# Kernel tuning notes

Hardware: AMD Instinct MI355X
Metric: run time of the kernel (lower is better)

## Reference

```python
import jax, jax.numpy as jnp
import numpy as np

N, M, D = 1024, 1024, 512


def setup_inputs() -> dict:
    key = jax.random.key(0)
    ks = jax.random.split(key, 12)
    s = 1.0 / np.sqrt(D)
    return {
        "q": jax.random.normal(ks[0], (N, D), jnp.float32),
        "k": jax.random.normal(ks[1], (M, D), jnp.float32),
        "v": jax.random.normal(ks[2], (M, D), jnp.float32),
        "mask": jax.random.randint(ks[3], (N, M), 0, 2) > 0,
        "Wq": jax.random.normal(ks[4], (D, D), jnp.float32) * s,
        "bq": jax.random.normal(ks[5], (D,), jnp.float32) * s,
        "Wk": jax.random.normal(ks[6], (D, D), jnp.float32) * s,
        "bk": jax.random.normal(ks[7], (D,), jnp.float32) * s,
        "Wv": jax.random.normal(ks[8], (D, D), jnp.float32) * s,
        "bv": jax.random.normal(ks[9], (D,), jnp.float32) * s,
        "Ww": jax.random.normal(ks[10], (D,), jnp.float32) * s,
        "bw": jax.random.normal(ks[11], (1,), jnp.float32) * s,
    }


def reference(q, k, v, mask, Wq, bq, Wk, bk, Wv, bv, Ww, bw):
    # Linear projections (torch Linear: x @ W.T + b)
    qp = q @ Wq.T + bq  # [N, D]
    kp = k @ Wk.T + bk  # [M, D]
    vp = v @ Wv.T + bv  # [M, D]
    # Bahdanau additive score: W(tanh(q_n + k_m)) -> [N, M]
    h = jnp.tanh(qp[:, None, :] + kp[None, :, :])  # [N, M, D]
    scores = jnp.einsum('nmd,d->nm', h, Ww) + bw[0]
    scores = jnp.where(mask, scores, jnp.float32(-1000000.0))
    attn = jax.nn.softmax(scores, axis=1)  # softmax over M (dim 1)
    context = jnp.einsum('nm,md->nd', attn, vp)  # [N, D]
    return context
```

## Files before the change

kernel.cpp:

```cpp
#include <hip/hip_runtime.h>
#include <hip/hip_bf16.h>
#include <float.h>


#define NROWS 1024
#define DDIM  512
#define MDIM  1024

typedef __attribute__((ext_vector_type(8))) short s8v;
typedef __attribute__((ext_vector_type(4))) float f4v;
typedef __attribute__((ext_vector_type(2))) float v2f;

__device__ __forceinline__ float bf2f(ushort h) {
    return __uint_as_float(((unsigned)h) << 16);
}
__device__ __forceinline__ ushort2 f2bf2(float a, float b) {
    __hip_bfloat162 t = __float22bfloat162_rn(float2{a, b});
    union { __hip_bfloat162 v; ushort2 u; } c; c.v = t;
    return c.u;
}
__device__ __forceinline__ void hl2(float a, float b, ushort2& h, ushort2& l) {
    h = f2bf2(a, b);
    l = f2bf2(a - bf2f(h.x), b - bf2f(h.y));
}

__global__ __launch_bounds__(256) void proj_gemm(
    const float* __restrict__ q, const float* __restrict__ kk_,
    const float* __restrict__ v,
    const float* __restrict__ Wq, const float* __restrict__ bq,
    const float* __restrict__ Wk, const float* __restrict__ bk,
    const float* __restrict__ Wv, const float* __restrict__ bv,
    float* __restrict__ eq, float* __restrict__ ekT,
    ushort* __restrict__ vph, ushort* __restrict__ vpl,
    float* __restrict__ rsum, float CS)
{
    __shared__ ushort Ah[4096], Al[4096], Bh[4096], Bl[4096];

    const float* A; const float* B; const float* bias;
    int biasRow;
    if (blockIdx.z == 0)      { A = q;   B = Wq;  bias = bq; biasRow = 0; }
    else if (blockIdx.z == 1) { A = Wk;  B = kk_; bias = bk; biasRow = 1; }
    else                      { A = Wv;  B = v;   bias = bv; biasRow = 1; }

    const int bi = (blockIdx.z == 0) ? blockIdx.x : blockIdx.y;
    const int bj = (blockIdx.z == 0) ? blockIdx.y : blockIdx.x;

    const int t    = threadIdx.x;
    const int lane = t & 63;
    const int w    = t >> 6;
    const int lm   = lane & 15;
    const int lq   = lane >> 4;
    const int i0   = bi * 64;
    const int j0   = bj * 64;
    const int mh   = (w >> 1) * 32;
    const int nh   = (w & 1) * 32;

    if (blockIdx.z == 0 && blockIdx.x == 0 && blockIdx.y == 0) {
        float4 zz = {0.f, 0.f, 0.f, 0.f};
        *(float4*)&rsum[t * 4] = zz;
    }

    f4v acc[2][2] = {{{0.f,0.f,0.f,0.f},{0.f,0.f,0.f,0.f}},
                     {{0.f,0.f,0.f,0.f},{0.f,0.f,0.f,0.f}}};
    float4 pa[4], pb[4];

    const int sr = t >> 4, sc4 = t & 15;
#pragma unroll
    for (int p = 0; p < 4; ++p) {
        int r = sr + p * 16;
        pa[p] = *(const float4*)&A[(size_t)(i0 + r) * DDIM + sc4 * 4];
        pb[p] = *(const float4*)&B[(size_t)(j0 + r) * DDIM + sc4 * 4];
    }

    for (int kc = 0; kc < 8; ++kc) {
        __syncthreads();
#pragma unroll
        for (int p = 0; p < 4; ++p) {
            int r = sr + p * 16;
            int ad = r * 64 + (((sc4 >> 1) ^ (r & 7)) << 3) + (sc4 & 1) * 4;
            ushort2 h01, l01, h23, l23;
            hl2(pa[p].x, pa[p].y, h01, l01);
            hl2(pa[p].z, pa[p].w, h23, l23);
            ushort4 ha = {h01.x, h01.y, h23.x, h23.y};
            ushort4 la = {l01.x, l01.y, l23.x, l23.y};
            *(ushort4*)&Ah[ad] = ha;
            *(ushort4*)&Al[ad] = la;
            hl2(pb[p].x, pb[p].y, h01, l01);
            hl2(pb[p].z, pb[p].w, h23, l23);
            ushort4 hb = {h01.x, h01.y, h23.x, h23.y};
            ushort4 lb = {l01.x, l01.y, l23.x, l23.y};
            *(ushort4*)&Bh[ad] = hb;
            *(ushort4*)&Bl[ad] = lb;
        }
        __syncthreads();
        if (kc < 7) {
            const int k0 = (kc + 1) * 64;
#pragma unroll
            for (int p = 0; p < 4; ++p) {
                int r = sr + p * 16;
                pa[p] = *(const float4*)&A[(size_t)(i0 + r) * DDIM + k0 + sc4 * 4];
                pb[p] = *(const float4*)&B[(size_t)(j0 + r) * DDIM + k0 + sc4 * 4];
            }
        }
#pragma unroll
        for (int ks = 0; ks < 2; ++ks) {
            const int kb = ks * 4 + lq;
            s8v afh[2], afl[2], bfh[2], bfl[2];
#pragma unroll
            for (int g = 0; g < 2; ++g) {
                int ra = mh + g * 16 + lm;
                int rb = nh + g * 16 + lm;
                int aa = ra * 64 + ((kb ^ (ra & 7)) << 3);
                int ab = rb * 64 + ((kb ^ (rb & 7)) << 3);
                afh[g] = *(const s8v*)&Ah[aa];
                afl[g] = *(const s8v*)&Al[aa];
                bfh[g] = *(const s8v*)&Bh[ab];
                bfl[g] = *(const s8v*)&Bl[ab];
            }
#pragma unroll
            for (int mi = 0; mi < 2; ++mi)
#pragma unroll
                for (int ni = 0; ni < 2; ++ni) {
                    acc[mi][ni] = __builtin_amdgcn_mfma_f32_16x16x32_bf16(
                        afh[mi], bfh[ni], acc[mi][ni], 0, 0, 0);
                    acc[mi][ni] = __builtin_amdgcn_mfma_f32_16x16x32_bf16(
                        afh[mi], bfl[ni], acc[mi][ni], 0, 0, 0);
                    acc[mi][ni] = __builtin_amdgcn_mfma_f32_16x16x32_bf16(
                        afl[mi], bfh[ni], acc[mi][ni], 0, 0, 0);
                }
        }
    }

    const float CLAMP = 8192.0f;
    const float SCw   = 1.220703125e-4f;
#pragma unroll
    for (int mi = 0; mi < 2; ++mi) {
#pragma unroll
        for (int ni = 0; ni < 2; ++ni) {
#pragma unroll
            for (int p = 0; p < 4; ++p) {
                int row = i0 + mh + mi * 16 + lq * 4 + p;
                int col = j0 + nh + ni * 16 + lm;
                float val = acc[mi][ni][p] + (biasRow ? bias[row] : bias[col]);
                if (blockIdx.z == 0) {
                    eq[(size_t)row * 512 + col] =
                        fminf(__builtin_amdgcn_exp2f(val * CS), CLAMP) * SCw;
                } else if (blockIdx.z == 1) {
                    ekT[(size_t)row * 1024 + col] =
                        fminf(__builtin_amdgcn_exp2f(val * CS), CLAMP);
                } else {
                    ushort2 h2 = f2bf2(val, val);
                    vph[(size_t)row * 1024 + col] = h2.x;
                    ushort2 l2 = f2bf2(val - bf2f(h2.x), 0.f);
                    vpl[(size_t)row * 1024 + col] = l2.x;
                }
            }
        }
    }
}


#define TREE8(K0,K1,K2,K3,K4,K5,K6,K7,DCQ)                                     \
    {                                                                          \
        float4 wgA = *(const float4*)&wws[(DCQ)];                              \
        float4 wgB = *(const float4*)&wws[(DCQ) + 4];                          \
        _Pragma("unroll")                                                      \
        for (int nn = 0; nn < 4; ++nn) {                                       \
            float4 egA = *(const float4*)&es[nn * 512 + (DCQ)];                \
            float4 egB = *(const float4*)&es[nn * 512 + (DCQ) + 4];            \
            v2f A0 = __builtin_elementwise_fma(K0, (v2f){egA.x, egA.x}, cc2);  \
            v2f A1 = __builtin_elementwise_fma(K1, (v2f){egA.y, egA.y}, cc2);  \
            v2f A2 = __builtin_elementwise_fma(K2, (v2f){egA.z, egA.z}, cc2);  \
            v2f A3 = __builtin_elementwise_fma(K3, (v2f){egA.w, egA.w}, cc2);  \
            v2f A4 = __builtin_elementwise_fma(K4, (v2f){egB.x, egB.x}, cc2);  \
            v2f A5 = __builtin_elementwise_fma(K5, (v2f){egB.y, egB.y}, cc2);  \
            v2f A6 = __builtin_elementwise_fma(K6, (v2f){egB.z, egB.z}, cc2);  \
            v2f A7 = __builtin_elementwise_fma(K7, (v2f){egB.w, egB.w}, cc2);  \
            v2f n01 = __builtin_elementwise_fma((v2f){wgA.y, wgA.y}, A0,       \
                                                (v2f){wgA.x, wgA.x} * A1);     \
            v2f d01 = A0 * A1;                                                 \
            v2f n23 = __builtin_elementwise_fma((v2f){wgA.w, wgA.w}, A2,       \
                                                (v2f){wgA.z, wgA.z} * A3);     \
            v2f d23 = A2 * A3;                                                 \
            v2f n45 = __builtin_elementwise_fma((v2f){wgB.y, wgB.y}, A4,       \
                                                (v2f){wgB.x, wgB.x} * A5);     \
            v2f d45 = A4 * A5;                                                 \
            v2f n67 = __builtin_elementwise_fma((v2f){wgB.w, wgB.w}, A6,       \
                                                (v2f){wgB.z, wgB.z} * A7);     \
            v2f d67 = A6 * A7;                                                 \
            v2f nA = __builtin_elementwise_fma(n01, d23, n23 * d01);           \
            v2f dA = d01 * d23;                                                \
            v2f nB = __builtin_elementwise_fma(n45, d67, n67 * d45);           \
            v2f dB = d45 * d67;                                                \
            v2f num = __builtin_elementwise_fma(nA, dB, nB * dA);              \
            v2f den = dA * dB;                                                 \
            v2f r = {__builtin_amdgcn_rcpf(den.x),                             \
                     __builtin_amdgcn_rcpf(den.y)};                            \
            acc[nn] = __builtin_elementwise_fma(num, r, acc[nn]);              \
        }                                                                      \
    }

__global__ __launch_bounds__(256) void score_kernel(const float* __restrict__ eq,
                                                    const float* __restrict__ ekT,
                                                    const float* __restrict__ Ww,
                                                    const int* __restrict__ mask,
                                                    ushort* __restrict__ Ph,
                                                    ushort* __restrict__ Pl,
                                                    float* __restrict__ rsum)
{
    __shared__ __align__(16) float es[4 * 512];
    __shared__ __align__(16) float wws[512];
    const int t    = threadIdx.x;
    const int lane = t & 63;
    const int w    = t >> 6;
    const int mw   = blockIdx.x * 512 + w * 128;
    const int n0   = blockIdx.y * 4;

    const float SC = 1.220703125e-4f;

#pragma unroll
    for (int p = 0; p < 2; ++p) {
        int idx = t + p * 256;
        int nl = idx >> 7, c4 = idx & 127;
        *(float4*)&es[nl * 512 + c4 * 4] =
            *(const float4*)&eq[(size_t)(n0 + nl) * DDIM + c4 * 4];
    }
    wws[t]       = Ww[t] * SC;
    wws[t + 256] = Ww[t + 256] * SC;

    const float* gk = ekT + mw + lane * 2;

    v2f a0 = *(const v2f*)(gk + (size_t)0 * MDIM);
    v2f a1 = *(const v2f*)(gk + (size_t)1 * MDIM);
    v2f a2 = *(const v2f*)(gk + (size_t)2 * MDIM);
    v2f a3 = *(const v2f*)(gk + (size_t)3 * MDIM);
    v2f a4 = *(const v2f*)(gk + (size_t)4 * MDIM);
    v2f a5 = *(const v2f*)(gk + (size_t)5 * MDIM);
    v2f a6 = *(const v2f*)(gk + (size_t)6 * MDIM);
    v2f a7 = *(const v2f*)(gk + (size_t)7 * MDIM);

    __syncthreads();

    v2f acc[4] = {};
    const v2f cc2 = {1.220703125e-4f, 1.220703125e-4f};

    for (int dc = 0; dc < 512; dc += 16) {
        const float* g8 = gk + (size_t)(dc + 8) * MDIM;
        v2f b0 = *(const v2f*)(g8 + (size_t)0 * MDIM);
        v2f b1 = *(const v2f*)(g8 + (size_t)1 * MDIM);
        v2f b2 = *(const v2f*)(g8 + (size_t)2 * MDIM);
        v2f b3 = *(const v2f*)(g8 + (size_t)3 * MDIM);
        v2f b4 = *(const v2f*)(g8 + (size_t)4 * MDIM);
        v2f b5 = *(const v2f*)(g8 + (size_t)5 * MDIM);
        v2f b6 = *(const v2f*)(g8 + (size_t)6 * MDIM);
        v2f b7 = *(const v2f*)(g8 + (size_t)7 * MDIM);

        TREE8(a0, a1, a2, a3, a4, a5, a6, a7, dc)

        if (dc + 16 < 512) {
            const float* g16 = gk + (size_t)(dc + 16) * MDIM;
            a0 = *(const v2f*)(g16 + (size_t)0 * MDIM);
            a1 = *(const v2f*)(g16 + (size_t)1 * MDIM);
            a2 = *(const v2f*)(g16 + (size_t)2 * MDIM);
            a3 = *(const v2f*)(g16 + (size_t)3 * MDIM);
            a4 = *(const v2f*)(g16 + (size_t)4 * MDIM);
            a5 = *(const v2f*)(g16 + (size_t)5 * MDIM);
            a6 = *(const v2f*)(g16 + (size_t)6 * MDIM);
            a7 = *(const v2f*)(g16 + (size_t)7 * MDIM);
        }

        TREE8(b0, b1, b2, b3, b4, b5, b6, b7, dc + 8)
    }

    const float C2 = -2.8853900817779268f;
    const int m = mw + lane * 2;
    float rs[4];
#pragma unroll
    for (int nn = 0; nn < 4; ++nn) {
        int n = n0 + nn;
        int2 mk = *(const int2*)&mask[(size_t)n * MDIM + m];
        float p0 = mk.x ? __builtin_amdgcn_exp2f(acc[nn].x * C2) : 0.f;
        float p1 = mk.y ? __builtin_amdgcn_exp2f(acc[nn].y * C2) : 0.f;
        ushort2 h, l;
        hl2(p0, p1, h, l);
        *(ushort2*)&Ph[(size_t)n * MDIM + m] = h;
        *(ushort2*)&Pl[(size_t)n * MDIM + m] = l;
        rs[nn] = p0 + p1;
    }
#pragma unroll
    for (int off = 32; off; off >>= 1) {
        rs[0] += __shfl_xor(rs[0], off);
        rs[1] += __shfl_xor(rs[1], off);
        rs[2] += __shfl_xor(rs[2], off);
        rs[3] += __shfl_xor(rs[3], off);
    }
    if (lane == 0) {
#pragma unroll
        for (int nn = 0; nn < 4; ++nn)
            atomicAdd(&rsum[n0 + nn], rs[nn]);
    }
}

__global__ __launch_bounds__(256) void ctx_gemm(const ushort* __restrict__ Ph,
                                                const ushort* __restrict__ Pl,
                                                const ushort* __restrict__ vph,
                                                const ushort* __restrict__ vpl,
                                                const float* __restrict__ rsum,
                                                float* __restrict__ out)
{
    __shared__ __align__(16) float red[3 * 64 * 4];
    const int t    = threadIdx.x;
    const int lane = t & 63;
    const int w    = t >> 6;
    const int lm   = lane & 15;
    const int lq   = lane >> 4;
    const int d0   = blockIdx.x * 16;
    const int n0   = blockIdx.y * 16;
    const int mb   = w * 256;

    const ushort* pAh = Ph  + (size_t)(n0 + lm) * MDIM + mb + lq * 8;
    const ushort* pAl = Pl  + (size_t)(n0 + lm) * MDIM + mb + lq * 8;
    const ushort* pBh = vph + (size_t)(d0 + lm) * MDIM + mb + lq * 8;
    const ushort* pBl = vpl + (size_t)(d0 + lm) * MDIM + mb + lq * 8;

    f4v acc = {0.f, 0.f, 0.f, 0.f};
#pragma unroll 4
    for (int m0 = 0; m0 < 256; m0 += 32) {
        s8v ah = *(const s8v*)(pAh + m0);
        s8v al = *(const s8v*)(pAl + m0);
        s8v bh = *(const s8v*)(pBh + m0);
        s8v bl = *(const s8v*)(pBl + m0);
        acc = __builtin_amdgcn_mfma_f32_16x16x32_bf16(ah, bh, acc, 0, 0, 0);
        acc = __builtin_amdgcn_mfma_f32_16x16x32_bf16(ah, bl, acc, 0, 0, 0);
        acc = __builtin_amdgcn_mfma_f32_16x16x32_bf16(al, bh, acc, 0, 0, 0);
    }

    if (w > 0) *(f4v*)&red[((w - 1) * 64 + lane) * 4] = acc;
    __syncthreads();
    if (w == 0) {
#pragma unroll
        for (int i = 0; i < 3; ++i)
            acc += *(const f4v*)&red[(i * 64 + lane) * 4];
#pragma unroll
        for (int p = 0; p < 4; ++p) {
            int nrow = n0 + lq * 4 + p;
            float inv = __builtin_amdgcn_rcpf(rsum[nrow]);
            out[(size_t)nrow * DDIM + d0 + lm] = acc[p] * inv;
        }
    }
}

extern "C" void kernel_launch(void* const* d_in, const int* in_sizes, int n_in,
                              void* d_out, int out_size, void* d_ws, size_t ws_size,
                              hipStream_t stream)
{
    const float* q    = (const float*)d_in[0];
    const float* k    = (const float*)d_in[1];
    const float* v    = (const float*)d_in[2];
    const int*   mask = (const int*)d_in[3];
    const float* Wq   = (const float*)d_in[4];
    const float* bq   = (const float*)d_in[5];
    const float* Wk   = (const float*)d_in[6];
    const float* bk   = (const float*)d_in[7];
    const float* Wv   = (const float*)d_in[8];
    const float* bv   = (const float*)d_in[9];
    const float* Ww   = (const float*)d_in[10];

    float* ws    = (float*)d_ws;
    float* eq    = ws;
    float* ekT   = ws + 524288;
    ushort* vph  = (ushort*)(ws + 1048576);
    ushort* vpl  = (ushort*)(ws + 1310720);
    ushort* Ph   = (ushort*)(ws + 1572864);
    ushort* Pl   = (ushort*)(ws + 2097152);
    float* rsum  = ws + 2621440;
    float* out   = (float*)d_out;

    const float CS = 2.8853900817779268f;

    proj_gemm<<<dim3(16, 8, 3), dim3(256), 0, stream>>>(q, k, v, Wq, bq, Wk, bk,
                                                        Wv, bv, eq, ekT,
                                                        vph, vpl, rsum, CS);
    score_kernel<<<dim3(2, 256), dim3(256), 0, stream>>>(eq, ekT, Ww, mask,
                                                         Ph, Pl, rsum);
    ctx_gemm<<<dim3(32, 64), dim3(256), 0, stream>>>(Ph, Pl, vph, vpl, rsum, out);
}
```

Measured before the change: 176.1 us.

## Split score kernel's D reduction across four wavefront groups with LDS reduce

The score kernel now uses 512-thread blocks in which eight waves cover two 128-wide M groups times four 128-wide D slices. Each wave reduces only its quarter of D, and partial accumulators are combined through shared memory before the masked exp, bf16 split and row-sum atomics. Grid width doubles to 4x256 blocks, raising the number of waves to hide latency on the long serial D loop. In exchange it adds an LDS reduction, a block barrier, and idle waves during the epilogue.

```diff
diff --git a/kernel.cpp b/kernel.cpp
--- a/kernel.cpp
+++ b/kernel.cpp
@@ -200,7 +200,7 @@
         }                                                                      \
     }
 
-__global__ __launch_bounds__(256) void score_kernel(const float* __restrict__ eq,
+__global__ __launch_bounds__(512) void score_kernel(const float* __restrict__ eq,
                                                     const float* __restrict__ ekT,
                                                     const float* __restrict__ Ww,
                                                     const int* __restrict__ mask,
@@ -210,25 +210,26 @@
 {
     __shared__ __align__(16) float es[4 * 512];
     __shared__ __align__(16) float wws[512];
+    __shared__ __align__(16) float red[3 * 2 * 64 * 8];
     const int t    = threadIdx.x;
     const int lane = t & 63;
     const int w    = t >> 6;
-    const int mw   = blockIdx.x * 512 + w * 128;
+    const int mg   = w & 1;
+    const int dh   = w >> 1;
+    const int mw   = blockIdx.x * 256 + mg * 128;
     const int n0   = blockIdx.y * 4;
+    const int db   = dh * 128;
 
     const float SC = 1.220703125e-4f;
 
-#pragma unroll
-    for (int p = 0; p < 2; ++p) {
-        int idx = t + p * 256;
-        int nl = idx >> 7, c4 = idx & 127;
+    {
+        int nl = t >> 7, c4 = t & 127;
         *(float4*)&es[nl * 512 + c4 * 4] =
             *(const float4*)&eq[(size_t)(n0 + nl) * DDIM + c4 * 4];
     }
-    wws[t]       = Ww[t] * SC;
-    wws[t + 256] = Ww[t + 256] * SC;
-
-    const float* gk = ekT + mw + lane * 2;
+    wws[t] = Ww[t] * SC;
+
+    const float* gk = ekT + (size_t)db * MDIM + mw + lane * 2;
 
     v2f a0 = *(const v2f*)(gk + (size_t)0 * MDIM);
     v2f a1 = *(const v2f*)(gk + (size_t)1 * MDIM);
@@ -244,7 +245,7 @@
     v2f acc[4] = {};
     const v2f cc2 = {1.220703125e-4f, 1.220703125e-4f};
 
-    for (int dc = 0; dc < 512; dc += 16) {
+    for (int dc = 0; dc < 128; dc += 16) {
         const float* g8 = gk + (size_t)(dc + 8) * MDIM;
         v2f b0 = *(const v2f*)(g8 + (size_t)0 * MDIM);
         v2f b1 = *(const v2f*)(g8 + (size_t)1 * MDIM);
@@ -255,9 +256,9 @@
         v2f b6 = *(const v2f*)(g8 + (size_t)6 * MDIM);
         v2f b7 = *(const v2f*)(g8 + (size_t)7 * MDIM);
 
-        TREE8(a0, a1, a2, a3, a4, a5, a6, a7, dc)
-
-        if (dc + 16 < 512) {
+        TREE8(a0, a1, a2, a3, a4, a5, a6, a7, db + dc)
+
+        if (dc + 16 < 128) {
             const float* g16 = gk + (size_t)(dc + 16) * MDIM;
             a0 = *(const v2f*)(g16 + (size_t)0 * MDIM);
             a1 = *(const v2f*)(g16 + (size_t)1 * MDIM);
@@ -269,35 +270,54 @@
             a7 = *(const v2f*)(g16 + (size_t)7 * MDIM);
         }
 
-        TREE8(b0, b1, b2, b3, b4, b5, b6, b7, dc + 8)
-    }
-
-    const float C2 = -2.8853900817779268f;
-    const int m = mw + lane * 2;
-    float rs[4];
-#pragma unroll
-    for (int nn = 0; nn < 4; ++nn) {
-        int n = n0 + nn;
-        int2 mk = *(const int2*)&mask[(size_t)n * MDIM + m];
-        float p0 = mk.x ? __builtin_amdgcn_exp2f(acc[nn].x * C2) : 0.f;
-        float p1 = mk.y ? __builtin_amdgcn_exp2f(acc[nn].y * C2) : 0.f;
-        ushort2 h, l;
-        hl2(p0, p1, h, l);
-        *(ushort2*)&Ph[(size_t)n * MDIM + m] = h;
-        *(ushort2*)&Pl[(size_t)n * MDIM + m] = l;
-        rs[nn] = p0 + p1;
-    }
-#pragma unroll
-    for (int off = 32; off; off >>= 1) {
-        rs[0] += __shfl_xor(rs[0], off);
-        rs[1] += __shfl_xor(rs[1], off);
-        rs[2] += __shfl_xor(rs[2], off);
-        rs[3] += __shfl_xor(rs[3], off);
-    }
-    if (lane == 0) {
-#pragma unroll
-        for (int nn = 0; nn < 4; ++nn)
-            atomicAdd(&rsum[n0 + nn], rs[nn]);
+        TREE8(b0, b1, b2, b3, b4, b5, b6, b7, db + dc + 8)
+    }
+
+    if (dh > 0) {
+        float* rb = &red[(((dh - 1) * 2 + mg) * 64 + lane) * 8];
+        *(v2f*)&rb[0] = acc[0];
+        *(v2f*)&rb[2] = acc[1];
+        *(v2f*)&rb[4] = acc[2];
+        *(v2f*)&rb[6] = acc[3];
+    }
+    __syncthreads();
+    if (dh == 0) {
+#pragma unroll
+        for (int i = 0; i < 3; ++i) {
+            const float* rb = &red[((i * 2 + mg) * 64 + lane) * 8];
+            acc[0] += *(const v2f*)&rb[0];
+            acc[1] += *(const v2f*)&rb[2];
+            acc[2] += *(const v2f*)&rb[4];
+            acc[3] += *(const v2f*)&rb[6];
+        }
+
+        const float C2 = -2.8853900817779268f;
+        const int m = mw + lane * 2;
+        float rs[4];
+#pragma unroll
+        for (int nn = 0; nn < 4; ++nn) {
+            int n = n0 + nn;
+            int2 mk = *(const int2*)&mask[(size_t)n * MDIM + m];
+            float p0 = mk.x ? __builtin_amdgcn_exp2f(acc[nn].x * C2) : 0.f;
+            float p1 = mk.y ? __builtin_amdgcn_exp2f(acc[nn].y * C2) : 0.f;
+            ushort2 h, l;
+            hl2(p0, p1, h, l);
+            *(ushort2*)&Ph[(size_t)n * MDIM + m] = h;
+            *(ushort2*)&Pl[(size_t)n * MDIM + m] = l;
+            rs[nn] = p0 + p1;
+        }
+#pragma unroll
+        for (int off = 32; off; off >>= 1) {
+            rs[0] += __shfl_xor(rs[0], off);
+            rs[1] += __shfl_xor(rs[1], off);
+            rs[2] += __shfl_xor(rs[2], off);
+            rs[3] += __shfl_xor(rs[3], off);
+        }
+        if (lane == 0) {
+#pragma unroll
+            for (int nn = 0; nn < 4; ++nn)
+                atomicAdd(&rsum[n0 + nn], rs[nn]);
+        }
     }
 }
 
@@ -381,7 +401,7 @@
     proj_gemm<<<dim3(16, 8, 3), dim3(256), 0, stream>>>(q, k, v, Wq, bq, Wk, bk,
                                                         Wv, bv, eq, ekT,
                                                         vph, vpl, rsum, CS);
-    score_kernel<<<dim3(2, 256), dim3(256), 0, stream>>>(eq, ekT, Ww, mask,
+    score_kernel<<<dim3(4, 256), dim3(512), 0, stream>>>(eq, ekT, Ww, mask,
                                                          Ph, Pl, rsum);
     ctx_gemm<<<dim3(32, 64), dim3(256), 0, stream>>>(Ph, Pl, vph, vpl, rsum, out);
 }
```

Result: no change. 177.3 us (+0.7%).

## Double-buffer LDS in projection GEMM and halve N-tile to double block count

Applied to the files above, without the earlier changes.

The projection GEMM now double-buffers its shared-memory tiles, with one barrier per k-chunk, and prefetches two chunks ahead so global loads and bf16 hi/lo splitting overlap with MFMA work. The output tile narrows from 64x64 to 64x32, which doubles the grid from 384 to 768 blocks to give more parallelism on the many CUs of the MI355X. The cost is more redundant reads of the A operand, fewer MFMAs per LDS load, and a larger LDS footprint per block.

```diff
diff --git a/kernel.cpp b/kernel.cpp
--- a/kernel.cpp
+++ b/kernel.cpp
@@ -34,7 +34,7 @@
     ushort* __restrict__ vph, ushort* __restrict__ vpl,
     float* __restrict__ rsum, float CS)
 {
-    __shared__ ushort Ah[4096], Al[4096], Bh[4096], Bl[4096];
+    __shared__ ushort Ah[2][4096], Al[2][4096], Bh[2][2048], Bl[2][2048];
 
     const float* A; const float* B; const float* bias;
     int biasRow;
@@ -42,8 +42,9 @@
     else if (blockIdx.z == 1) { A = Wk;  B = kk_; bias = bk; biasRow = 1; }
     else                      { A = Wv;  B = v;   bias = bv; biasRow = 1; }
 
-    const int bi = (blockIdx.z == 0) ? blockIdx.x : blockIdx.y;
-    const int bj = (blockIdx.z == 0) ? blockIdx.y : blockIdx.x;
+    const int bx = blockIdx.x;
+    const int bi = (blockIdx.z == 0) ? (bx >> 4) : (bx >> 5);
+    const int bj = (blockIdx.z == 0) ? (bx & 15) : (bx & 31);
 
     const int t    = threadIdx.x;
     const int lane = t & 63;
@@ -51,84 +52,103 @@
     const int lm   = lane & 15;
     const int lq   = lane >> 4;
     const int i0   = bi * 64;
-    const int j0   = bj * 64;
+    const int j0   = bj * 32;
     const int mh   = (w >> 1) * 32;
-    const int nh   = (w & 1) * 32;
-
-    if (blockIdx.z == 0 && blockIdx.x == 0 && blockIdx.y == 0) {
+    const int nh   = (w & 1) * 16;
+
+    if (blockIdx.z == 0 && bx == 0) {
         float4 zz = {0.f, 0.f, 0.f, 0.f};
         *(float4*)&rsum[t * 4] = zz;
     }
 
-    f4v acc[2][2] = {{{0.f,0.f,0.f,0.f},{0.f,0.f,0.f,0.f}},
-                     {{0.f,0.f,0.f,0.f},{0.f,0.f,0.f,0.f}}};
-    float4 pa[4], pb[4];
-
     const int sr = t >> 4, sc4 = t & 15;
-#pragma unroll
-    for (int p = 0; p < 4; ++p) {
-        int r = sr + p * 16;
-        pa[p] = *(const float4*)&A[(size_t)(i0 + r) * DDIM + sc4 * 4];
-        pb[p] = *(const float4*)&B[(size_t)(j0 + r) * DDIM + sc4 * 4];
-    }
+
+    float4 pa[4], pb[2];
+
+#define LOAD_CHUNK(KC)                                                         \
+    {                                                                          \
+        const int k0 = (KC) * 64;                                              \
+        _Pragma("unroll")                                                      \
+        for (int p = 0; p < 4; ++p)                                            \
+            pa[p] = *(const float4*)&A[(size_t)(i0 + sr + p * 16) * DDIM       \
+                                       + k0 + sc4 * 4];                        \
+        _Pragma("unroll")                                                      \
+        for (int p = 0; p < 2; ++p)                                            \
+            pb[p] = *(const float4*)&B[(size_t)(j0 + sr + p * 16) * DDIM       \
+                                       + k0 + sc4 * 4];                        \
+    }
+
+#define WRITE_CHUNK(BUF)                                                       \
+    {                                                                          \
+        _Pragma("unroll")                                                      \
+        for (int p = 0; p < 4; ++p) {                                          \
+            int r = sr + p * 16;                                               \
+            int ad = r * 64 + (((sc4 >> 1) ^ (r & 7)) << 3) + (sc4 & 1) * 4;   \
+            ushort2 h01, l01, h23, l23;                                        \
+            hl2(pa[p].x, pa[p].y, h01, l01);                                   \
+            hl2(pa[p].z, pa[p].w, h23, l23);                                   \
+            ushort4 ha = {h01.x, h01.y, h23.x, h23.y};                         \
+            ushort4 la = {l01.x, l01.y, l23.x, l23.y};                         \
+            *(ushort4*)&Ah[BUF][ad] = ha;                                      \
+            *(ushort4*)&Al[BUF][ad] = la;                                      \
+        }                                                                      \
+        _Pragma("unroll")                                                      \
+        for (int p = 0; p < 2; ++p) {                                          \
+            int r = sr + p * 16;                                               \
+            int ad = r * 64 + (((sc4 >> 1) ^ (r & 7)) << 3) + (sc4 & 1) * 4;   \
+            ushort2 h01, l01, h23, l23;                                        \
+            hl2(pb[p].x, pb[p].y, h01, l01);                                   \
+            hl2(pb[p].z, pb[p].w, h23, l23);                                   \
+            ushort4 hb = {h01.x, h01.y, h23.x, h23.y};                         \
+            ushort4 lb = {l01.x, l01.y, l23.x, l23.y};                         \
+            *(ushort4*)&Bh[BUF][ad] = hb;                                      \
+            *(ushort4*)&Bl[BUF][ad] = lb;                                      \
+        }                                                                      \
+    }
+
+    f4v acc[2] = {{0.f,0.f,0.f,0.f},{0.f,0.f,0.f,0.f}};
+
+    LOAD_CHUNK(0)
+    WRITE_CHUNK(0)
+    LOAD_CHUNK(1)
+    __syncthreads();
 
     for (int kc = 0; kc < 8; ++kc) {
-        __syncthreads();
-#pragma unroll
-        for (int p = 0; p < 4; ++p) {
-            int r = sr + p * 16;
-            int ad = r * 64 + (((sc4 >> 1) ^ (r & 7)) << 3) + (sc4 & 1) * 4;
-            ushort2 h01, l01, h23, l23;
-            hl2(pa[p].x, pa[p].y, h01, l01);
-            hl2(pa[p].z, pa[p].w, h23, l23);
-            ushort4 ha = {h01.x, h01.y, h23.x, h23.y};
-            ushort4 la = {l01.x, l01.y, l23.x, l23.y};
-            *(ushort4*)&Ah[ad] = ha;
-            *(ushort4*)&Al[ad] = la;
-            hl2(pb[p].x, pb[p].y, h01, l01);
-            hl2(pb[p].z, pb[p].w, h23, l23);
-            ushort4 hb = {h01.x, h01.y, h23.x, h23.y};
-            ushort4 lb = {l01.x, l01.y, l23.x, l23.y};
-            *(ushort4*)&Bh[ad] = hb;
-            *(ushort4*)&Bl[ad] = lb;
-        }
-        __syncthreads();
-        if (kc < 7) {
-            const int k0 = (kc + 1) * 64;
-#pragma unroll
-            for (int p = 0; p < 4; ++p) {
-                int r = sr + p * 16;
-                pa[p] = *(const float4*)&A[(size_t)(i0 + r) * DDIM + k0 + sc4 * 4];
-                pb[p] = *(const float4*)&B[(size_t)(j0 + r) * DDIM + k0 + sc4 * 4];
-            }
-        }
+        const int buf = kc & 1;
 #pragma unroll
         for (int ks = 0; ks < 2; ++ks) {
             const int kb = ks * 4 + lq;
-            s8v afh[2], afl[2], bfh[2], bfl[2];
+            s8v afh[2], afl[2], bfh, bfl;
 #pragma unroll
             for (int g = 0; g < 2; ++g) {
                 int ra = mh + g * 16 + lm;
-                int rb = nh + g * 16 + lm;
                 int aa = ra * 64 + ((kb ^ (ra & 7)) << 3);
+                afh[g] = *(const s8v*)&Ah[buf][aa];
+                afl[g] = *(const s8v*)&Al[buf][aa];
+            }
+            {
+                int rb = nh + lm;
                 int ab = rb * 64 + ((kb ^ (rb & 7)) << 3);
-                afh[g] = *(const s8v*)&Ah[aa];
-                afl[g] = *(const s8v*)&Al[aa];
-                bfh[g] = *(const s8v*)&Bh[ab];
-                bfl[g] = *(const s8v*)&Bl[ab];
+                bfh = *(const s8v*)&Bh[buf][ab];
+                bfl = *(const s8v*)&Bl[buf][ab];
             }
 #pragma unroll
-            for (int mi = 0; mi < 2; ++mi)
-#pragma unroll
-                for (int ni = 0; ni < 2; ++ni) {
-                    acc[mi][ni] = __builtin_amdgcn_mfma_f32_16x16x32_bf16(
-                        afh[mi], bfh[ni], acc[mi][ni], 0, 0, 0);
-                    acc[mi][ni] = __builtin_amdgcn_mfma_f32_16x16x32_bf16(
-                        afh[mi], bfl[ni], acc[mi][ni], 0, 0, 0);
-                    acc[mi][ni] = __builtin_amdgcn_mfma_f32_16x16x32_bf16(
-                        afl[mi], bfh[ni], acc[mi][ni], 0, 0, 0);
-                }
-        }
+            for (int mi = 0; mi < 2; ++mi) {
+                acc[mi] = __builtin_amdgcn_mfma_f32_16x16x32_bf16(
+                    afh[mi], bfh, acc[mi], 0, 0, 0);
+                acc[mi] = __builtin_amdgcn_mfma_f32_16x16x32_bf16(
+                    afh[mi], bfl, acc[mi], 0, 0, 0);
+                acc[mi] = __builtin_amdgcn_mfma_f32_16x16x32_bf16(
+                    afl[mi], bfh, acc[mi], 0, 0, 0);
+            }
+        }
+        if (kc < 7) {
+            WRITE_CHUNK(buf ^ 1)
+        }
+        if (kc < 6) {
+            LOAD_CHUNK(kc + 2)
+        }
+        __syncthreads();
     }
 
     const float CLAMP = 8192.0f;
@@ -136,27 +156,26 @@
 #pragma unroll
     for (int mi = 0; mi < 2; ++mi) {
 #pragma unroll
-        for (int ni = 0; ni < 2; ++ni) {
-#pragma unroll
-            for (int p = 0; p < 4; ++p) {
-                int row = i0 + mh + mi * 16 + lq * 4 + p;
-                int col = j0 + nh + ni * 16 + lm;
-                float val = acc[mi][ni][p] + (biasRow ? bias[row] : bias[col]);
-                if (blockIdx.z == 0) {
-                    eq[(size_t)row * 512 + col] =
-                        fminf(__builtin_amdgcn_exp2f(val * CS), CLAMP) * SCw;
-                } else if (blockIdx.z == 1) {
-                    ekT[(size_t)row * 1024 + col] =
-                        fminf(__builtin_amdgcn_exp2f(val * CS), CLAMP);
-                } else {
-                    ushort2 h2 = f2bf2(val, val);
-                    vph[(size_t)row * 1024 + col] = h2.x;
-                    ushort2 l2 = f2bf2(val - bf2f(h2.x), 0.f);
-                    vpl[(size_t)row * 1024 + col] = l2.x;
-                }
+        for (int p = 0; p < 4; ++p) {
+            int row = i0 + mh + mi * 16 + lq * 4 + p;
+            int col = j0 + nh + lm;
+            float val = acc[mi][p] + (biasRow ? bias[row] : bias[col]);
+            if (blockIdx.z == 0) {
+                eq[(size_t)row * 512 + col] =
+                    fminf(__builtin_amdgcn_exp2f(val * CS), CLAMP) * SCw;
+            } else if (blockIdx.z == 1) {
+                ekT[(size_t)row * 1024 + col] =
+                    fminf(__builtin_amdgcn_exp2f(val * CS), CLAMP);
+            } else {
+                ushort2 h2 = f2bf2(val, val);
+                vph[(size_t)row * 1024 + col] = h2.x;
+                ushort2 l2 = f2bf2(val - bf2f(h2.x), 0.f);
+                vpl[(size_t)row * 1024 + col] = l2.x;
             }
         }
     }
+#undef LOAD_CHUNK
+#undef WRITE_CHUNK
 }
 
 
@@ -378,9 +397,9 @@
 
     const float CS = 2.8853900817779268f;
 
-    proj_gemm<<<dim3(16, 8, 3), dim3(256), 0, stream>>>(q, k, v, Wq, bq, Wk, bk,
-                                                        Wv, bv, eq, ekT,
-                                                        vph, vpl, rsum, CS);
+    proj_gemm<<<dim3(256, 1, 3), dim3(256), 0, stream>>>(q, k, v, Wq, bq, Wk, bk,
+                                                         Wv, bv, eq, ekT,
+                                                         vph, vpl, rsum, CS);
     score_kernel<<<dim3(2, 256), dim3(256), 0, stream>>>(eq, ekT, Ww, mask,
                                                          Ph, Pl, rsum);
     ctx_gemm<<<dim3(32, 64), dim3(256), 0, stream>>>(Ph, Pl, vph, vpl, rsum, out);
```

After: 175.8 us. About the same (-0.2%).
